# Optimization experiments

Measured on AMD Instinct MI355X. Metric: run time of the kernel, lower is better.

Reference implementation:

```python
import jax, jax.numpy as jnp
import numpy as np
import math

B, L, D, H = 4, 1024, 1024, 16
HD = D // H

def setup_inputs() -> dict:
    rng = jax.random.key(0)
    ks = jax.random.split(rng, 11)
    def lin(k):
        # orthogonal-ish init not needed for numerics; normal scaled like torch default
        return jax.random.normal(k, (D, D), dtype=jnp.float32) * 0.02
    return {
        'key':   jax.random.normal(ks[0], (B, L, D), dtype=jnp.float32),
        'value': jax.random.normal(ks[1], (B, L, D), dtype=jnp.float32),
        'query': jax.random.normal(ks[2], (B, L, D), dtype=jnp.float32),
        'Wk': lin(ks[3]), 'bk': jnp.zeros((D,), jnp.float32),
        'Wq': lin(ks[4]), 'bq': jnp.zeros((D,), jnp.float32),
        'Wv': lin(ks[5]), 'bv': jnp.zeros((D,), jnp.float32),
        'Wp': lin(ks[6]), 'bp': jnp.zeros((D,), jnp.float32),
    }

def reference(key, value, query, Wk, bk, Wq, bq, Wv, bv, Wp, bp):
    # linear projections (torch Linear: x @ W.T + b)
    k = (key   @ Wk.T + bk).reshape(B, L, H, HD).transpose(0, 2, 1, 3)  # [B,H,L,hd]
    q = (query @ Wq.T + bq).reshape(B, L, H, HD).transpose(0, 2, 1, 3)
    v = (value @ Wv.T + bv).reshape(B, L, H, HD).transpose(0, 2, 1, 3)
    att = jnp.einsum('bhqd,bhkd->bhqk', q, k) * (1.0 / math.sqrt(HD))  # [B,H,L,L]
    causal = jnp.tril(jnp.ones((L, L), dtype=bool))
    att = jnp.where(causal[None, None], att, -jnp.inf)
    att = jax.nn.softmax(att, axis=-1)
    y = jnp.einsum('bhqk,bhkd->bhqd', att, v)  # [B,H,L,hd]
    y = y.transpose(0, 2, 1, 3).reshape(B, L, D)
    return y @ Wp.T + bp
```

## Files before the change

### kernel.cpp

```cpp
#include <hip/hip_runtime.h>

typedef unsigned short u16;
typedef __attribute__((ext_vector_type(8))) short bf16x8;
typedef __attribute__((ext_vector_type(4))) float f32x4;
typedef __attribute__((ext_vector_type(4))) unsigned short u16x4;

#define MFMA16 __builtin_amdgcn_mfma_f32_16x16x32_bf16

__device__ inline u16 f2bf(float f) {
    union { float f; unsigned u; } v; v.f = f;
    return (u16)((v.u + 0x8000u) >> 16);
}

__device__ inline void gld16(const u16* g, u16* l) {
    __builtin_amdgcn_global_load_lds(
        (const __attribute__((address_space(1))) unsigned int*)g,
        (__attribute__((address_space(3))) unsigned int*)l, 16, 0, 0);
}

struct CvtArgs { const float* src[7]; u16* dst[7]; };

__global__ __launch_bounds__(256) void cvt_kernel(CvtArgs a) {
    const int z = blockIdx.z;
    const int n = (z < 3) ? 4194304 : 1048576;
    const size_t i = ((size_t)blockIdx.x * 256 + threadIdx.x) * 8;
    if (i >= (size_t)n) return;
    const float* s = a.src[z];
    float4 v0 = *(const float4*)(s + i);
    float4 v1 = *(const float4*)(s + i + 4);
    union { u16 h[8]; bf16x8 v; } o;
    o.h[0] = f2bf(v0.x); o.h[1] = f2bf(v0.y); o.h[2] = f2bf(v0.z); o.h[3] = f2bf(v0.w);
    o.h[4] = f2bf(v1.x); o.h[5] = f2bf(v1.y); o.h[6] = f2bf(v1.z); o.h[7] = f2bf(v1.w);
    *(bf16x8*)(a.dst[z] + i) = o.v;
}

struct GemmArgs { const u16* A; const u16* W; const float* bias; void* out; int epi; };
struct Gemm3Args { GemmArgs g[3]; };

__global__ __launch_bounds__(256, 3) void gemm_qkv(Gemm3Args ga) {
    __shared__ u16 lA[128 * 64];
    __shared__ u16 lB[128 * 64];
    const GemmArgs g = ga.g[blockIdx.z];
    const int t = threadIdx.x, wave = t >> 6, lane = t & 63;
    const int quad = lane >> 4, l16 = lane & 15;
    const int rowsA = blockIdx.y * 128, rowsB = blockIdx.x * 128;
    const int wm = (wave >> 1) * 64, wn = (wave & 1) * 64;
    const u16* A = g.A; const u16* W = g.W;

    f32x4 acc[4][4] = {};

    for (int kb = 0; kb < 1024; kb += 64) {
#pragma unroll
        for (int i = 0; i < 4; i++) {
            int u = (i * 4 + wave) * 64 + lane;
            int row = u >> 3, cu = (u & 7) ^ (row & 7);
            gld16(A + (size_t)(rowsA + row) * 1024 + kb + cu * 8, lA + u * 8);
        }
#pragma unroll
        for (int i = 0; i < 4; i++) {
            int u = (i * 4 + wave) * 64 + lane;
            int row = u >> 3, cu = (u & 7) ^ (row & 7);
            gld16(W + (size_t)(rowsB + row) * 1024 + kb + cu * 8, lB + u * 8);
        }
        __syncthreads();

        bf16x8 af[4][2], bfr[4][2];
#pragma unroll
        for (int mi = 0; mi < 4; mi++) {
            int row = wm + mi * 16 + l16;
#pragma unroll
            for (int kr = 0; kr < 2; kr++)
                af[mi][kr] = *(const bf16x8*)(lA + row * 64 + (((kr * 4 + quad) ^ (row & 7)) * 8));
        }
#pragma unroll
        for (int ni = 0; ni < 4; ni++) {
            int row = wn + ni * 16 + l16;
#pragma unroll
            for (int kr = 0; kr < 2; kr++)
                bfr[ni][kr] = *(const bf16x8*)(lB + row * 64 + (((kr * 4 + quad) ^ (row & 7)) * 8));
        }
#pragma unroll
        for (int mi = 0; mi < 4; mi++)
#pragma unroll
            for (int ni = 0; ni < 4; ni++) {
                acc[mi][ni] = MFMA16(af[mi][0], bfr[ni][0], acc[mi][ni], 0, 0, 0);
                acc[mi][ni] = MFMA16(af[mi][1], bfr[ni][1], acc[mi][ni], 0, 0, 0);
            }
        __syncthreads();
    }

    const int epi = g.epi;
#pragma unroll
    for (int ni = 0; ni < 4; ni++) {
        const int ncol = rowsB + wn + ni * 16 + l16;
        const float bv = g.bias[ncol];
        const int h = ncol >> 6, hd = ncol & 63;
#pragma unroll
        for (int mi = 0; mi < 4; mi++) {
            const int mrow0 = rowsA + wm + mi * 16 + quad * 4;
            const int b = mrow0 >> 10, l0 = mrow0 & 1023;
            if (epi == 0) {
#pragma unroll
                for (int r = 0; r < 4; r++)
                    ((u16*)g.out)[((size_t)(b * 16 + h) * 1024 + l0 + r) * 64 + hd] =
                        f2bf(acc[mi][ni][r] + bv);
            } else {
                u16x4 pk;
#pragma unroll
                for (int r = 0; r < 4; r++) pk[r] = f2bf(acc[mi][ni][r] + bv);
                *(u16x4*)((u16*)g.out + ((size_t)(b * 16 + h) * 64 + hd) * 1024 + l0) = pk;
            }
        }
    }
}

__global__ __launch_bounds__(256, 2) void gemm_p(const u16* __restrict__ A,
                                                 const u16* __restrict__ W,
                                                 const float* __restrict__ bias,
                                                 float* __restrict__ out)
{
    __shared__ u16 lA[128 * 64];
    __shared__ u16 lB[64 * 64];
    const int t = threadIdx.x, wave = t >> 6, lane = t & 63;
    const int quad = lane >> 4, l16 = lane & 15;
    const int rowsA = blockIdx.y * 128, rowsB = blockIdx.x * 64;
    const int wm = (wave >> 1) * 64, wn = (wave & 1) * 32;

    f32x4 acc[4][2] = {};

    for (int kb = 0; kb < 1024; kb += 64) {
#pragma unroll
        for (int i = 0; i < 4; i++) {
            int u = (i * 4 + wave) * 64 + lane;
            int row = u >> 3, cu = (u & 7) ^ (row & 7);
            gld16(A + (size_t)(rowsA + row) * 1024 + kb + cu * 8, lA + u * 8);
        }
#pragma unroll
        for (int i = 0; i < 2; i++) {
            int u = (i * 4 + wave) * 64 + lane;
            int row = u >> 3, cu = (u & 7) ^ (row & 7);
            gld16(W + (size_t)(rowsB + row) * 1024 + kb + cu * 8, lB + u * 8);
        }
        __syncthreads();

        bf16x8 af[4][2], bfr[2][2];
#pragma unroll
        for (int mi = 0; mi < 4; mi++) {
            int row = wm + mi * 16 + l16;
#pragma unroll
            for (int kr = 0; kr < 2; kr++)
                af[mi][kr] = *(const bf16x8*)(lA + row * 64 + (((kr * 4 + quad) ^ (row & 7)) * 8));
        }
#pragma unroll
        for (int ni = 0; ni < 2; ni++) {
            int row = wn + ni * 16 + l16;
#pragma unroll
            for (int kr = 0; kr < 2; kr++)
                bfr[ni][kr] = *(const bf16x8*)(lB + row * 64 + (((kr * 4 + quad) ^ (row & 7)) * 8));
        }
#pragma unroll
        for (int mi = 0; mi < 4; mi++)
#pragma unroll
            for (int ni = 0; ni < 2; ni++) {
                acc[mi][ni] = MFMA16(af[mi][0], bfr[ni][0], acc[mi][ni], 0, 0, 0);
                acc[mi][ni] = MFMA16(af[mi][1], bfr[ni][1], acc[mi][ni], 0, 0, 0);
            }
        __syncthreads();
    }

#pragma unroll
    for (int ni = 0; ni < 2; ni++) {
        const int ncol = rowsB + wn + ni * 16 + l16;
        const float bv = bias[ncol];
#pragma unroll
        for (int mi = 0; mi < 4; mi++) {
            const int mrow0 = rowsA + wm + mi * 16 + quad * 4;
#pragma unroll
            for (int r = 0; r < 4; r++)
                out[(size_t)(mrow0 + r) * 1024 + ncol] = acc[mi][ni][r] + bv;
        }
    }
}

__global__ __launch_bounds__(256) void attn_kernel(const u16* __restrict__ qh,
                                                   const u16* __restrict__ kh,
                                                   const u16* __restrict__ vhT,
                                                   u16* __restrict__ y)
{
    __shared__ u16 sK[64 * 64];
    __shared__ u16 sVT[64 * 64];
    __shared__ u16 sP[4 * 16 * 72];

    const int t = threadIdx.x, wave = t >> 6, lane = t & 63;
    const int quad = lane >> 4, l16 = lane & 15;
    const int p = blockIdx.x, bh = blockIdx.y;
    const int qt0 = 15 - p, qt1 = p;
    const size_t base = (size_t)bh * 1024 * 64;
    const float e2 = 0.18033688f;

    bf16x8 aq[2][2];
#pragma unroll
    for (int s = 0; s < 2; s++) {
        const int qoff = (s == 0 ? qt0 : qt1) * 64 + wave * 16;
#pragma unroll
        for (int kr = 0; kr < 2; kr++)
            aq[s][kr] = *(const bf16x8*)(qh + base + (size_t)(qoff + l16) * 64 + kr * 32 + quad * 8);
    }

    bf16x8 ones;
#pragma unroll
    for (int j = 0; j < 8; j++) ones[j] = (short)0x3F80;

    f32x4 o[2][4] = {};
    f32x4 lacc[2] = {};
    u16* pw = sP + wave * 16 * 72;

    for (int kb = 0; kb <= qt0; kb++) {
        const int krow0 = kb * 64;
#pragma unroll
        for (int i = 0; i < 2; i++) {
            int u = (i * 4 + wave) * 64 + lane;
            int row = u >> 3, cu = (u & 7) ^ (row & 7);
            gld16(kh + base + (size_t)(krow0 + row) * 64 + cu * 8, sK + u * 8);
        }
#pragma unroll
        for (int i = 0; i < 2; i++) {
            int u = (i * 4 + wave) * 64 + lane;
            int row = u >> 3, cu = (u & 7) ^ (row & 7);
            gld16(vhT + ((size_t)(bh * 64 + row)) * 1024 + krow0 + cu * 8, sVT + u * 8);
        }
        __syncthreads();

        bf16x8 bk[4][2], bv[4][2];
#pragma unroll
        for (int kc = 0; kc < 4; kc++) {
            int row = kc * 16 + l16;
#pragma unroll
            for (int kr = 0; kr < 2; kr++)
                bk[kc][kr] = *(const bf16x8*)(sK + row * 64 + (((kr * 4 + quad) ^ (row & 7)) * 8));
        }
#pragma unroll
        for (int nt = 0; nt < 4; nt++) {
            int row = nt * 16 + l16;
#pragma unroll
            for (int kr = 0; kr < 2; kr++)
                bv[nt][kr] = *(const bf16x8*)(sVT + row * 64 + (((kr * 4 + quad) ^ (row & 7)) * 8));
        }

        auto compute = [&](int s, int qtv) {
            const int qoff = qtv * 64 + wave * 16;
            f32x4 sc[4];
#pragma unroll
            for (int kc = 0; kc < 4; kc++) {
                f32x4 z = {};
                z = MFMA16(aq[s][0], bk[kc][0], z, 0, 0, 0);
                z = MFMA16(aq[s][1], bk[kc][1], z, 0, 0, 0);
                sc[kc] = z;
            }
            const bool diag = (kb == qtv);
#pragma unroll
            for (int kc = 0; kc < 4; kc++)
#pragma unroll
                for (int r = 0; r < 4; r++) {
                    float x = fminf(sc[kc][r] * e2, 43.f);
                    float pv = exp2f(x);
                    if (diag) {
                        int kcol = krow0 + kc * 16 + l16;
                        int qrow = qoff + quad * 4 + r;
                        if (kcol > qrow) pv = 0.f;
                    }
                    pw[(quad * 4 + r) * 72 + kc * 16 + l16] = f2bf(pv);
                }
            bf16x8 ap0 = *(const bf16x8*)(pw + l16 * 72 + quad * 8);
            bf16x8 ap1 = *(const bf16x8*)(pw + l16 * 72 + 32 + quad * 8);
#pragma unroll
            for (int nt = 0; nt < 4; nt++) {
                o[s][nt] = MFMA16(ap0, bv[nt][0], o[s][nt], 0, 0, 0);
                o[s][nt] = MFMA16(ap1, bv[nt][1], o[s][nt], 0, 0, 0);
            }
            lacc[s] = MFMA16(ap0, ones, lacc[s], 0, 0, 0);
            lacc[s] = MFMA16(ap1, ones, lacc[s], 0, 0, 0);
        };

        compute(0, qt0);
        if (kb <= qt1) compute(1, qt1);
        __syncthreads();
    }

    const int b = bh >> 4, h = bh & 15;
#pragma unroll
    for (int s = 0; s < 2; s++) {
        const int qoff = (s == 0 ? qt0 : qt1) * 64 + wave * 16;
#pragma unroll
        for (int nt = 0; nt < 4; nt++)
#pragma unroll
            for (int r = 0; r < 4; r++) {
                int qrow = qoff + quad * 4 + r;
                int d = nt * 16 + l16;
                y[(size_t)(b * 1024 + qrow) * 1024 + h * 64 + d] =
                    f2bf(o[s][nt][r] / lacc[s][r]);
            }
    }
}

extern "C" void kernel_launch(void* const* d_in, const int* in_sizes, int n_in,
                              void* d_out, int out_size, void* d_ws, size_t ws_size,
                              hipStream_t stream)
{
    const float* key   = (const float*)d_in[0];
    const float* value = (const float*)d_in[1];
    const float* query = (const float*)d_in[2];
    const float* Wk = (const float*)d_in[3];
    const float* bk = (const float*)d_in[4];
    const float* Wq = (const float*)d_in[5];
    const float* bq = (const float*)d_in[6];
    const float* Wv = (const float*)d_in[7];
    const float* bv = (const float*)d_in[8];
    const float* Wp = (const float*)d_in[9];
    const float* bp = (const float*)d_in[10];

    char* ws = (char*)d_ws;
    u16* xq  = (u16*)(ws + (size_t)( 0 << 20));
    u16* xk  = (u16*)(ws + (size_t)( 8 << 20));
    u16* xv  = (u16*)(ws + (size_t)(16 << 20));
    u16* wqb = (u16*)(ws + (size_t)(24 << 20));
    u16* wkb = (u16*)(ws + (size_t)(26 << 20));
    u16* wvb = (u16*)(ws + (size_t)(28 << 20));
    u16* wpb = (u16*)(ws + (size_t)(30 << 20));
    u16* qh  = (u16*)(ws + (size_t)(32 << 20));
    u16* kh  = (u16*)(ws + (size_t)(40 << 20));
    u16* vhT = (u16*)(ws + (size_t)(48 << 20));
    u16* y   = xq;

    CvtArgs ca;
    ca.src[0] = query; ca.dst[0] = xq;
    ca.src[1] = key;   ca.dst[1] = xk;
    ca.src[2] = value; ca.dst[2] = xv;
    ca.src[3] = Wq;    ca.dst[3] = wqb;
    ca.src[4] = Wk;    ca.dst[4] = wkb;
    ca.src[5] = Wv;    ca.dst[5] = wvb;
    ca.src[6] = Wp;    ca.dst[6] = wpb;
    hipLaunchKernelGGL(cvt_kernel, dim3(2048, 1, 7), dim3(256), 0, stream, ca);

    Gemm3Args g3;
    g3.g[0] = GemmArgs{xq, wqb, bq, (void*)qh,  0};
    g3.g[1] = GemmArgs{xk, wkb, bk, (void*)kh,  0};
    g3.g[2] = GemmArgs{xv, wvb, bv, (void*)vhT, 2};
    hipLaunchKernelGGL(gemm_qkv, dim3(8, 32, 3), dim3(256), 0, stream, g3);

    hipLaunchKernelGGL(attn_kernel, dim3(8, 64), dim3(256), 0, stream, qh, kh, vhT, y);

    hipLaunchKernelGGL(gemm_p, dim3(16, 32), dim3(256), 0, stream, y, wpb, bp, (float*)d_out);
}
```

Baseline: 203.9 us.

## Split-K output projection with atomics and restructure attention into 128-row query tiles

The output projection GEMM now uses 128x128 tiles with a 2-way split over K, accumulating into the fp32 output via atomicAdd. The output is zeroed by an extra slice of the conversion kernel. The attention kernel drops the paired-tile load balancing and gives each block one 128-row query tile, with each wave owning 32 query rows (two 16-row fragments). Diagonal masking and work skipping are done per fragment. This aims for more MFMA work per K/V load and better GEMM tile reuse, at the cost of atomic traffic, non-deterministic summation order and less balanced causal work across blocks.

```diff
diff --git a/kernel.cpp b/kernel.cpp
--- a/kernel.cpp
+++ b/kernel.cpp
@@ -18,12 +18,18 @@
         (__attribute__((address_space(3))) unsigned int*)l, 16, 0, 0);
 }
 
-struct CvtArgs { const float* src[7]; u16* dst[7]; };
+struct CvtArgs { const float* src[7]; u16* dst[7]; float* zero; };
 
 __global__ __launch_bounds__(256) void cvt_kernel(CvtArgs a) {
     const int z = blockIdx.z;
+    const size_t i = ((size_t)blockIdx.x * 256 + threadIdx.x) * 8;
+    if (z == 7) {
+        float4 zz = {0.f, 0.f, 0.f, 0.f};
+        *(float4*)(a.zero + i) = zz;
+        *(float4*)(a.zero + i + 4) = zz;
+        return;
+    }
     const int n = (z < 3) ? 4194304 : 1048576;
-    const size_t i = ((size_t)blockIdx.x * 256 + threadIdx.x) * 8;
     if (i >= (size_t)n) return;
     const float* s = a.src[z];
     float4 v0 = *(const float4*)(s + i);
@@ -114,21 +120,22 @@
     }
 }
 
-__global__ __launch_bounds__(256, 2) void gemm_p(const u16* __restrict__ A,
+__global__ __launch_bounds__(256, 3) void gemm_p(const u16* __restrict__ A,
                                                  const u16* __restrict__ W,
                                                  const float* __restrict__ bias,
                                                  float* __restrict__ out)
 {
     __shared__ u16 lA[128 * 64];
-    __shared__ u16 lB[64 * 64];
+    __shared__ u16 lB[128 * 64];
     const int t = threadIdx.x, wave = t >> 6, lane = t & 63;
     const int quad = lane >> 4, l16 = lane & 15;
-    const int rowsA = blockIdx.y * 128, rowsB = blockIdx.x * 64;
-    const int wm = (wave >> 1) * 64, wn = (wave & 1) * 32;
-
-    f32x4 acc[4][2] = {};
-
-    for (int kb = 0; kb < 1024; kb += 64) {
+    const int rowsA = blockIdx.y * 128, rowsB = blockIdx.x * 128;
+    const int wm = (wave >> 1) * 64, wn = (wave & 1) * 64;
+    const int k0 = blockIdx.z * 512;
+
+    f32x4 acc[4][4] = {};
+
+    for (int kb = k0; kb < k0 + 512; kb += 64) {
 #pragma unroll
         for (int i = 0; i < 4; i++) {
             int u = (i * 4 + wave) * 64 + lane;
@@ -136,14 +143,14 @@
             gld16(A + (size_t)(rowsA + row) * 1024 + kb + cu * 8, lA + u * 8);
         }
 #pragma unroll
-        for (int i = 0; i < 2; i++) {
+        for (int i = 0; i < 4; i++) {
             int u = (i * 4 + wave) * 64 + lane;
             int row = u >> 3, cu = (u & 7) ^ (row & 7);
             gld16(W + (size_t)(rowsB + row) * 1024 + kb + cu * 8, lB + u * 8);
         }
         __syncthreads();
 
-        bf16x8 af[4][2], bfr[2][2];
+        bf16x8 af[4][2], bfr[4][2];
 #pragma unroll
         for (int mi = 0; mi < 4; mi++) {
             int row = wm + mi * 16 + l16;
@@ -152,7 +159,7 @@
                 af[mi][kr] = *(const bf16x8*)(lA + row * 64 + (((kr * 4 + quad) ^ (row & 7)) * 8));
         }
 #pragma unroll
-        for (int ni = 0; ni < 2; ni++) {
+        for (int ni = 0; ni < 4; ni++) {
             int row = wn + ni * 16 + l16;
 #pragma unroll
             for (int kr = 0; kr < 2; kr++)
@@ -161,51 +168,50 @@
 #pragma unroll
         for (int mi = 0; mi < 4; mi++)
 #pragma unroll
-            for (int ni = 0; ni < 2; ni++) {
+            for (int ni = 0; ni < 4; ni++) {
                 acc[mi][ni] = MFMA16(af[mi][0], bfr[ni][0], acc[mi][ni], 0, 0, 0);
                 acc[mi][ni] = MFMA16(af[mi][1], bfr[ni][1], acc[mi][ni], 0, 0, 0);
             }
         __syncthreads();
     }
 
-#pragma unroll
-    for (int ni = 0; ni < 2; ni++) {
+    const bool addb = (blockIdx.z == 0);
+#pragma unroll
+    for (int ni = 0; ni < 4; ni++) {
         const int ncol = rowsB + wn + ni * 16 + l16;
-        const float bv = bias[ncol];
+        const float bv = addb ? bias[ncol] : 0.f;
 #pragma unroll
         for (int mi = 0; mi < 4; mi++) {
             const int mrow0 = rowsA + wm + mi * 16 + quad * 4;
 #pragma unroll
             for (int r = 0; r < 4; r++)
-                out[(size_t)(mrow0 + r) * 1024 + ncol] = acc[mi][ni][r] + bv;
-        }
-    }
-}
-
-__global__ __launch_bounds__(256) void attn_kernel(const u16* __restrict__ qh,
-                                                   const u16* __restrict__ kh,
-                                                   const u16* __restrict__ vhT,
-                                                   u16* __restrict__ y)
+                atomicAdd(&out[(size_t)(mrow0 + r) * 1024 + ncol], acc[mi][ni][r] + bv);
+        }
+    }
+}
+
+__global__ __launch_bounds__(256, 3) void attn_kernel(const u16* __restrict__ qh,
+                                                      const u16* __restrict__ kh,
+                                                      const u16* __restrict__ vhT,
+                                                      u16* __restrict__ y)
 {
     __shared__ u16 sK[64 * 64];
     __shared__ u16 sVT[64 * 64];
-    __shared__ u16 sP[4 * 16 * 72];
+    __shared__ u16 sP[4 * 32 * 72];
 
     const int t = threadIdx.x, wave = t >> 6, lane = t & 63;
     const int quad = lane >> 4, l16 = lane & 15;
-    const int p = blockIdx.x, bh = blockIdx.y;
-    const int qt0 = 15 - p, qt1 = p;
+    const int qt = 7 - blockIdx.x, bh = blockIdx.y;
     const size_t base = (size_t)bh * 1024 * 64;
+    const int qoff = qt * 128 + wave * 32;
     const float e2 = 0.18033688f;
 
     bf16x8 aq[2][2];
 #pragma unroll
-    for (int s = 0; s < 2; s++) {
-        const int qoff = (s == 0 ? qt0 : qt1) * 64 + wave * 16;
+    for (int qf = 0; qf < 2; qf++)
 #pragma unroll
         for (int kr = 0; kr < 2; kr++)
-            aq[s][kr] = *(const bf16x8*)(qh + base + (size_t)(qoff + l16) * 64 + kr * 32 + quad * 8);
-    }
+            aq[qf][kr] = *(const bf16x8*)(qh + base + (size_t)(qoff + qf * 16 + l16) * 64 + kr * 32 + quad * 8);
 
     bf16x8 ones;
 #pragma unroll
@@ -213,9 +219,10 @@
 
     f32x4 o[2][4] = {};
     f32x4 lacc[2] = {};
-    u16* pw = sP + wave * 16 * 72;
-
-    for (int kb = 0; kb <= qt0; kb++) {
+    u16* pw = sP + wave * 32 * 72;
+
+    const int nkb = 2 * qt + 2;
+    for (int kb = 0; kb < nkb; kb++) {
         const int krow0 = kb * 64;
 #pragma unroll
         for (int i = 0; i < 2; i++) {
@@ -231,7 +238,7 @@
         }
         __syncthreads();
 
-        bf16x8 bk[4][2], bv[4][2];
+        bf16x8 bk[4][2];
 #pragma unroll
         for (int kc = 0; kc < 4; kc++) {
             int row = kc * 16 + l16;
@@ -239,6 +246,44 @@
             for (int kr = 0; kr < 2; kr++)
                 bk[kc][kr] = *(const bf16x8*)(sK + row * 64 + (((kr * 4 + quad) ^ (row & 7)) * 8));
         }
+
+        f32x4 sc[2][4];
+        bool act[2];
+#pragma unroll
+        for (int qf = 0; qf < 2; qf++) {
+            const int qbase = qoff + qf * 16;
+            act[qf] = (krow0 <= qbase + 15);
+            if (act[qf]) {
+#pragma unroll
+                for (int kc = 0; kc < 4; kc++) {
+                    f32x4 z = {};
+                    z = MFMA16(aq[qf][0], bk[kc][0], z, 0, 0, 0);
+                    z = MFMA16(aq[qf][1], bk[kc][1], z, 0, 0, 0);
+                    sc[qf][kc] = z;
+                }
+            }
+        }
+#pragma unroll
+        for (int qf = 0; qf < 2; qf++) {
+            if (!act[qf]) continue;
+            const int qbase = qoff + qf * 16;
+            const bool dm = (krow0 + 63 > qbase);
+#pragma unroll
+            for (int kc = 0; kc < 4; kc++)
+#pragma unroll
+                for (int r = 0; r < 4; r++) {
+                    float x = fminf(sc[qf][kc][r] * e2, 43.f);
+                    float pv = exp2f(x);
+                    if (dm) {
+                        int kcol = krow0 + kc * 16 + l16;
+                        int qrow = qbase + quad * 4 + r;
+                        if (kcol > qrow) pv = 0.f;
+                    }
+                    pw[(qf * 16 + quad * 4 + r) * 72 + kc * 16 + l16] = f2bf(pv);
+                }
+        }
+
+        bf16x8 bv[4][2];
 #pragma unroll
         for (int nt = 0; nt < 4; nt++) {
             int row = nt * 16 + l16;
@@ -246,61 +291,34 @@
             for (int kr = 0; kr < 2; kr++)
                 bv[nt][kr] = *(const bf16x8*)(sVT + row * 64 + (((kr * 4 + quad) ^ (row & 7)) * 8));
         }
-
-        auto compute = [&](int s, int qtv) {
-            const int qoff = qtv * 64 + wave * 16;
-            f32x4 sc[4];
-#pragma unroll
-            for (int kc = 0; kc < 4; kc++) {
-                f32x4 z = {};
-                z = MFMA16(aq[s][0], bk[kc][0], z, 0, 0, 0);
-                z = MFMA16(aq[s][1], bk[kc][1], z, 0, 0, 0);
-                sc[kc] = z;
-            }
-            const bool diag = (kb == qtv);
-#pragma unroll
-            for (int kc = 0; kc < 4; kc++)
-#pragma unroll
-                for (int r = 0; r < 4; r++) {
-                    float x = fminf(sc[kc][r] * e2, 43.f);
-                    float pv = exp2f(x);
-                    if (diag) {
-                        int kcol = krow0 + kc * 16 + l16;
-                        int qrow = qoff + quad * 4 + r;
-                        if (kcol > qrow) pv = 0.f;
-                    }
-                    pw[(quad * 4 + r) * 72 + kc * 16 + l16] = f2bf(pv);
-                }
-            bf16x8 ap0 = *(const bf16x8*)(pw + l16 * 72 + quad * 8);
-            bf16x8 ap1 = *(const bf16x8*)(pw + l16 * 72 + 32 + quad * 8);
+#pragma unroll
+        for (int qf = 0; qf < 2; qf++) {
+            if (!act[qf]) continue;
+            bf16x8 ap0 = *(const bf16x8*)(pw + (qf * 16 + l16) * 72 + quad * 8);
+            bf16x8 ap1 = *(const bf16x8*)(pw + (qf * 16 + l16) * 72 + 32 + quad * 8);
 #pragma unroll
             for (int nt = 0; nt < 4; nt++) {
-                o[s][nt] = MFMA16(ap0, bv[nt][0], o[s][nt], 0, 0, 0);
-                o[s][nt] = MFMA16(ap1, bv[nt][1], o[s][nt], 0, 0, 0);
-            }
-            lacc[s] = MFMA16(ap0, ones, lacc[s], 0, 0, 0);
-            lacc[s] = MFMA16(ap1, ones, lacc[s], 0, 0, 0);
-        };
-
-        compute(0, qt0);
-        if (kb <= qt1) compute(1, qt1);
+                o[qf][nt] = MFMA16(ap0, bv[nt][0], o[qf][nt], 0, 0, 0);
+                o[qf][nt] = MFMA16(ap1, bv[nt][1], o[qf][nt], 0, 0, 0);
+            }
+            lacc[qf] = MFMA16(ap0, ones, lacc[qf], 0, 0, 0);
+            lacc[qf] = MFMA16(ap1, ones, lacc[qf], 0, 0, 0);
+        }
         __syncthreads();
     }
 
     const int b = bh >> 4, h = bh & 15;
 #pragma unroll
-    for (int s = 0; s < 2; s++) {
-        const int qoff = (s == 0 ? qt0 : qt1) * 64 + wave * 16;
+    for (int qf = 0; qf < 2; qf++)
 #pragma unroll
         for (int nt = 0; nt < 4; nt++)
 #pragma unroll
             for (int r = 0; r < 4; r++) {
-                int qrow = qoff + quad * 4 + r;
+                int qrow = qoff + qf * 16 + quad * 4 + r;
                 int d = nt * 16 + l16;
                 y[(size_t)(b * 1024 + qrow) * 1024 + h * 64 + d] =
-                    f2bf(o[s][nt][r] / lacc[s][r]);
-            }
-    }
+                    f2bf(o[qf][nt][r] / lacc[qf][r]);
+            }
 }
 
 extern "C" void kernel_launch(void* const* d_in, const int* in_sizes, int n_in,
@@ -340,7 +358,8 @@
     ca.src[4] = Wk;    ca.dst[4] = wkb;
     ca.src[5] = Wv;    ca.dst[5] = wvb;
     ca.src[6] = Wp;    ca.dst[6] = wpb;
-    hipLaunchKernelGGL(cvt_kernel, dim3(2048, 1, 7), dim3(256), 0, stream, ca);
+    ca.zero = (float*)d_out;
+    hipLaunchKernelGGL(cvt_kernel, dim3(2048, 1, 8), dim3(256), 0, stream, ca);
 
     Gemm3Args g3;
     g3.g[0] = GemmArgs{xq, wqb, bq, (void*)qh,  0};
@@ -350,5 +369,5 @@
 
     hipLaunchKernelGGL(attn_kernel, dim3(8, 64), dim3(256), 0, stream, qh, kh, vhT, y);
 
-    hipLaunchKernelGGL(gemm_p, dim3(16, 32), dim3(256), 0, stream, y, wpb, bp, (float*)d_out);
-}
+    hipLaunchKernelGGL(gemm_p, dim3(8, 32, 2), dim3(256), 0, stream, y, wpb, bp, (float*)d_out);
+}
```

New measurement: 242.4 us. 18.9% more time.

## Remap GEMM tiles for XCD locality and split attention into finer balanced chunks

Applied to the files above, without the earlier changes.

The QKV and output-projection GEMMs now use a 1D grid, with block IDs remapped so that blocks sharing an M tile land on the same XCD (bid&7), which is meant to improve L2 reuse. The attention kernel now splits query work into 32-row chunks and pairs a long chunk with a short chunk across the two wave-pairs of each block, doubling the grid to 16x64 blocks. It also adds launch bounds of 4 for higher occupancy and skips compute for K tiles past a wave's causal range. In exchange, each K/V tile loaded is used by fewer query rows, so more global traffic is spent per output.

```diff
diff --git a/kernel.cpp b/kernel.cpp
--- a/kernel.cpp
+++ b/kernel.cpp
@@ -43,7 +43,10 @@
     const GemmArgs g = ga.g[blockIdx.z];
     const int t = threadIdx.x, wave = t >> 6, lane = t & 63;
     const int quad = lane >> 4, l16 = lane & 15;
-    const int rowsA = blockIdx.y * 128, rowsB = blockIdx.x * 128;
+    const int bid = blockIdx.x;
+    const int mtile = (bid & 7) * 4 + (bid >> 6);
+    const int ntile = (bid >> 3) & 7;
+    const int rowsA = mtile * 128, rowsB = ntile * 128;
     const int wm = (wave >> 1) * 64, wn = (wave & 1) * 64;
     const u16* A = g.A; const u16* W = g.W;
 
@@ -123,7 +126,10 @@
     __shared__ u16 lB[64 * 64];
     const int t = threadIdx.x, wave = t >> 6, lane = t & 63;
     const int quad = lane >> 4, l16 = lane & 15;
-    const int rowsA = blockIdx.y * 128, rowsB = blockIdx.x * 64;
+    const int bid = blockIdx.x;
+    const int mtile = (bid & 7) * 4 + (bid >> 7);
+    const int ntile = (bid >> 3) & 15;
+    const int rowsA = mtile * 128, rowsB = ntile * 64;
     const int wm = (wave >> 1) * 64, wn = (wave & 1) * 32;
 
     f32x4 acc[4][2] = {};
@@ -182,10 +188,10 @@
     }
 }
 
-__global__ __launch_bounds__(256) void attn_kernel(const u16* __restrict__ qh,
-                                                   const u16* __restrict__ kh,
-                                                   const u16* __restrict__ vhT,
-                                                   u16* __restrict__ y)
+__global__ __launch_bounds__(256, 4) void attn_kernel(const u16* __restrict__ qh,
+                                                      const u16* __restrict__ kh,
+                                                      const u16* __restrict__ vhT,
+                                                      u16* __restrict__ y)
 {
     __shared__ u16 sK[64 * 64];
     __shared__ u16 sVT[64 * 64];
@@ -194,28 +200,27 @@
     const int t = threadIdx.x, wave = t >> 6, lane = t & 63;
     const int quad = lane >> 4, l16 = lane & 15;
     const int p = blockIdx.x, bh = blockIdx.y;
-    const int qt0 = 15 - p, qt1 = p;
+    const int c_l = 31 - p;
+    const int chunk = (wave < 2) ? c_l : p;
+    const int qbase = chunk * 32 + (wave & 1) * 16;
     const size_t base = (size_t)bh * 1024 * 64;
     const float e2 = 0.18033688f;
 
-    bf16x8 aq[2][2];
-#pragma unroll
-    for (int s = 0; s < 2; s++) {
-        const int qoff = (s == 0 ? qt0 : qt1) * 64 + wave * 16;
-#pragma unroll
-        for (int kr = 0; kr < 2; kr++)
-            aq[s][kr] = *(const bf16x8*)(qh + base + (size_t)(qoff + l16) * 64 + kr * 32 + quad * 8);
-    }
+    bf16x8 aq[2];
+#pragma unroll
+    for (int kr = 0; kr < 2; kr++)
+        aq[kr] = *(const bf16x8*)(qh + base + (size_t)(qbase + l16) * 64 + kr * 32 + quad * 8);
 
     bf16x8 ones;
 #pragma unroll
     for (int j = 0; j < 8; j++) ones[j] = (short)0x3F80;
 
-    f32x4 o[2][4] = {};
-    f32x4 lacc[2] = {};
+    f32x4 o[4] = {};
+    f32x4 lacc = {};
     u16* pw = sP + wave * 16 * 72;
 
-    for (int kb = 0; kb <= qt0; kb++) {
+    const int nkb = (c_l + 2) >> 1;
+    for (int kb = 0; kb < nkb; kb++) {
         const int krow0 = kb * 64;
 #pragma unroll
         for (int i = 0; i < 2; i++) {
@@ -231,76 +236,67 @@
         }
         __syncthreads();
 
-        bf16x8 bk[4][2], bv[4][2];
-#pragma unroll
-        for (int kc = 0; kc < 4; kc++) {
-            int row = kc * 16 + l16;
-#pragma unroll
-            for (int kr = 0; kr < 2; kr++)
-                bk[kc][kr] = *(const bf16x8*)(sK + row * 64 + (((kr * 4 + quad) ^ (row & 7)) * 8));
-        }
-#pragma unroll
-        for (int nt = 0; nt < 4; nt++) {
-            int row = nt * 16 + l16;
-#pragma unroll
-            for (int kr = 0; kr < 2; kr++)
-                bv[nt][kr] = *(const bf16x8*)(sVT + row * 64 + (((kr * 4 + quad) ^ (row & 7)) * 8));
-        }
-
-        auto compute = [&](int s, int qtv) {
-            const int qoff = qtv * 64 + wave * 16;
+        if (krow0 <= qbase + 15) {
+            bf16x8 bk[4][2];
+#pragma unroll
+            for (int kc = 0; kc < 4; kc++) {
+                int row = kc * 16 + l16;
+#pragma unroll
+                for (int kr = 0; kr < 2; kr++)
+                    bk[kc][kr] = *(const bf16x8*)(sK + row * 64 + (((kr * 4 + quad) ^ (row & 7)) * 8));
+            }
             f32x4 sc[4];
 #pragma unroll
             for (int kc = 0; kc < 4; kc++) {
                 f32x4 z = {};
-                z = MFMA16(aq[s][0], bk[kc][0], z, 0, 0, 0);
-                z = MFMA16(aq[s][1], bk[kc][1], z, 0, 0, 0);
+                z = MFMA16(aq[0], bk[kc][0], z, 0, 0, 0);
+                z = MFMA16(aq[1], bk[kc][1], z, 0, 0, 0);
                 sc[kc] = z;
             }
-            const bool diag = (kb == qtv);
+            const bool dm = (krow0 + 63 > qbase);
 #pragma unroll
             for (int kc = 0; kc < 4; kc++)
 #pragma unroll
                 for (int r = 0; r < 4; r++) {
                     float x = fminf(sc[kc][r] * e2, 43.f);
                     float pv = exp2f(x);
-                    if (diag) {
+                    if (dm) {
                         int kcol = krow0 + kc * 16 + l16;
-                        int qrow = qoff + quad * 4 + r;
+                        int qrow = qbase + quad * 4 + r;
                         if (kcol > qrow) pv = 0.f;
                     }
                     pw[(quad * 4 + r) * 72 + kc * 16 + l16] = f2bf(pv);
                 }
+            bf16x8 bv[4][2];
+#pragma unroll
+            for (int nt = 0; nt < 4; nt++) {
+                int row = nt * 16 + l16;
+#pragma unroll
+                for (int kr = 0; kr < 2; kr++)
+                    bv[nt][kr] = *(const bf16x8*)(sVT + row * 64 + (((kr * 4 + quad) ^ (row & 7)) * 8));
+            }
             bf16x8 ap0 = *(const bf16x8*)(pw + l16 * 72 + quad * 8);
             bf16x8 ap1 = *(const bf16x8*)(pw + l16 * 72 + 32 + quad * 8);
 #pragma unroll
             for (int nt = 0; nt < 4; nt++) {
-                o[s][nt] = MFMA16(ap0, bv[nt][0], o[s][nt], 0, 0, 0);
-                o[s][nt] = MFMA16(ap1, bv[nt][1], o[s][nt], 0, 0, 0);
-            }
-            lacc[s] = MFMA16(ap0, ones, lacc[s], 0, 0, 0);
-            lacc[s] = MFMA16(ap1, ones, lacc[s], 0, 0, 0);
-        };
-
-        compute(0, qt0);
-        if (kb <= qt1) compute(1, qt1);
+                o[nt] = MFMA16(ap0, bv[nt][0], o[nt], 0, 0, 0);
+                o[nt] = MFMA16(ap1, bv[nt][1], o[nt], 0, 0, 0);
+            }
+            lacc = MFMA16(ap0, ones, lacc, 0, 0, 0);
+            lacc = MFMA16(ap1, ones, lacc, 0, 0, 0);
+        }
         __syncthreads();
     }
 
     const int b = bh >> 4, h = bh & 15;
 #pragma unroll
-    for (int s = 0; s < 2; s++) {
-        const int qoff = (s == 0 ? qt0 : qt1) * 64 + wave * 16;
-#pragma unroll
-        for (int nt = 0; nt < 4; nt++)
-#pragma unroll
-            for (int r = 0; r < 4; r++) {
-                int qrow = qoff + quad * 4 + r;
-                int d = nt * 16 + l16;
-                y[(size_t)(b * 1024 + qrow) * 1024 + h * 64 + d] =
-                    f2bf(o[s][nt][r] / lacc[s][r]);
-            }
-    }
+    for (int nt = 0; nt < 4; nt++)
+#pragma unroll
+        for (int r = 0; r < 4; r++) {
+            int qrow = qbase + quad * 4 + r;
+            int d = nt * 16 + l16;
+            y[(size_t)(b * 1024 + qrow) * 1024 + h * 64 + d] = f2bf(o[nt][r] / lacc[r]);
+        }
 }
 
 extern "C" void kernel_launch(void* const* d_in, const int* in_sizes, int n_in,
@@ -346,9 +342,9 @@
     g3.g[0] = GemmArgs{xq, wqb, bq, (void*)qh,  0};
     g3.g[1] = GemmArgs{xk, wkb, bk, (void*)kh,  0};
     g3.g[2] = GemmArgs{xv, wvb, bv, (void*)vhT, 2};
-    hipLaunchKernelGGL(gemm_qkv, dim3(8, 32, 3), dim3(256), 0, stream, g3);
-
-    hipLaunchKernelGGL(attn_kernel, dim3(8, 64), dim3(256), 0, stream, qh, kh, vhT, y);
-
-    hipLaunchKernelGGL(gemm_p, dim3(16, 32), dim3(256), 0, stream, y, wpb, bp, (float*)d_out);
-}
+    hipLaunchKernelGGL(gemm_qkv, dim3(256, 1, 3), dim3(256), 0, stream, g3);
+
+    hipLaunchKernelGGL(attn_kernel, dim3(16, 64), dim3(256), 0, stream, qh, kh, vhT, y);
+
+    hipLaunchKernelGGL(gemm_p, dim3(512), dim3(256), 0, stream, y, wpb, bp, (float*)d_out);
+}
```

After: 197.0 us. 3.4% less time.
